# Performance work log

Measured on AMD Instinct MI355X. Metric: run time of the kernel, lower is better.

## Reference

```python
import jax, jax.numpy as jnp
import numpy as np

B, J, D, H, W, AE, GH, NA, EH, L = 64, 20000, 32, 64, 4, 16, 24, 5000, 128, 32


def _ln(x, g=None, b=None, eps=1e-5):
    mu = x.mean(-1, keepdims=True)
    var = jnp.mean((x - mu) ** 2, axis=-1, keepdims=True)
    y = (x - mu) * jax.lax.rsqrt(var + eps)
    if g is not None:
        y = y * g + b
    return y


def setup_inputs():
    key = jax.random.key(0)
    ks = jax.random.split(key, 12)
    def rn(k, shape, s):
        return (jax.random.normal(k, shape) * s).astype(jnp.float32)
    return {
        "x": jax.random.normal(ks[0], (B, J), jnp.float32),
        "mask": jax.random.randint(ks[1], (B, J), 0, 2, jnp.int32),
        "atse_idx": jax.random.randint(ks[2], (J,), 0, NA, jnp.int32),
        "feature_embedding": jax.random.normal(ks[3], (J, D), jnp.float32),
        "atse_embedding": jax.random.normal(ks[4], (NA, AE), jnp.float32),
        "h_W1": rn(ks[5], (1 + D, H), 0.15), "h_b1": jnp.zeros((H,), jnp.float32),
        "h_ln1_g": jnp.ones((H,), jnp.float32), "h_ln1_b": jnp.zeros((H,), jnp.float32),
        "h_W2": rn(ks[6], (H, D), 0.12), "h_b2": jnp.zeros((D,), jnp.float32),
        "h_ln2_g": jnp.ones((D,), jnp.float32), "h_ln2_b": jnp.zeros((D,), jnp.float32),
        "g_W1": rn(ks[7], (D + AE, GH), 0.14), "g_b1": jnp.zeros((GH,), jnp.float32),
        "g_W2": rn(ks[8], (GH, W), 0.2), "g_b2": jnp.zeros((W,), jnp.float32),
        "c_W": rn(ks[9], (W * D, D), 0.09), "c_b": jnp.zeros((D,), jnp.float32),
        "c_ln_g": jnp.ones((D,), jnp.float32), "c_ln_b": jnp.zeros((D,), jnp.float32),
        "e_W1": rn(ks[10], (D, EH), 0.18), "e_b1": jnp.zeros((EH,), jnp.float32),
        "e_W2": rn(ks[11], (EH, 2 * L), 0.09), "e_b2": jnp.zeros((2 * L,), jnp.float32),
    }


def _forward(x, mask, atse_idx, feature_embedding, atse_embedding,
             h_W1, h_b1, h_ln1_g, h_ln1_b, h_W2, h_b2, h_ln2_g, h_ln2_b,
             g_W1, g_b1, g_W2, g_b2, c_W, c_b, c_ln_g, c_ln_b,
             e_W1, e_b1, e_W2, e_b2):
    TEMP = 1.0  # temperature_fixed=True -> scale = temperature_value
    Bv, Jv = x.shape
    Dv = feature_embedding.shape[1]
    # h-layer on all (b, j) pairs; LayerNorm/ReLU are per-row so this equals the
    # per-sample gather version on observed rows (unobserved rows get zero weight below).
    h_in = jnp.concatenate(
        [x[..., None], jnp.broadcast_to(feature_embedding[None], (Bv, Jv, Dv))], axis=-1)
    h = jax.nn.relu(_ln(h_in @ h_W1 + h_b1, h_ln1_g, h_ln1_b))
    h_out = jax.nn.relu(_ln(h @ h_W2 + h_b2, h_ln2_g, h_ln2_b))  # [B, J, D]
    # gate: [h_out | E_atse(j)] -> W head logits
    ae = atse_embedding[atse_idx]  # [J, AE]
    gate_in = jnp.concatenate(
        [h_out, jnp.broadcast_to(ae[None], (Bv, Jv, ae.shape[1]))], axis=-1)
    raw = jax.nn.relu(gate_in @ g_W1 + g_b1) @ g_W2 + g_b2  # [B, J, W]
    logits = jnp.clip(raw * TEMP, -10.0, 10.0)
    obs = mask.astype(bool)
    masked = jnp.where(obs[..., None], logits, -1e9)
    weights = jax.nn.softmax(masked, axis=1)  # softmax over observed junctions per head
    head_sums = jnp.einsum('bjw,bjd->bwd', weights, h_out)  # [B, W, D]
    Wn, Dn = head_sums.shape[1], head_sums.shape[2]
    combined = jax.nn.relu(_ln(head_sums.reshape(Bv, Wn * Dn) @ c_W + c_b, c_ln_g, c_ln_b))
    combined = jnp.where(obs.any(axis=1)[:, None], combined, 0.0)  # empty-mask rows -> zeros
    # encoder_mlp: scvi FCLayers, 2 layers, LayerNorm (no affine) + ReLU each
    e1 = jax.nn.relu(_ln(combined @ e_W1 + e_b1))
    mu_logvar = jax.nn.relu(_ln(e1 @ e_W2 + e_b2))
    mu, logvar = jnp.split(mu_logvar, 2, axis=-1)
    return mu, logvar


def reference(x, mask, atse_idx, feature_embedding, atse_embedding,
              h_W1, h_b1, h_ln1_g, h_ln1_b, h_W2, h_b2, h_ln2_g, h_ln2_b,
              g_W1, g_b1, g_W2, g_b2, c_W, c_b, c_ln_g, c_ln_b,
              e_W1, e_b1, e_W2, e_b2):
    return _forward(x, mask, atse_idx, feature_embedding, atse_embedding,
                    h_W1, h_b1, h_ln1_g, h_ln1_b, h_W2, h_b2, h_ln2_g, h_ln2_b,
                    g_W1, g_b1, g_W2, g_b2, c_W, c_b, c_ln_g, c_ln_b,
                    e_W1, e_b1, e_W2, e_b2)
```

## Files before the change

### kernel.cpp

```cpp
#include <hip/hip_runtime.h>
#include <hip/hip_bf16.h>
#include <math.h>

#define Bv 64
#define Jv 20000
#define NJT 625
#define NBT 8

typedef __attribute__((ext_vector_type(8))) short short8;
typedef __attribute__((ext_vector_type(4))) float f32x4;

union U8 { short8 s; unsigned int u[4]; };

__device__ __forceinline__ unsigned short f2bf(float f) {
  unsigned int u = __float_as_uint(f);
  u += 0x7FFFu + ((u >> 16) & 1u);
  return (unsigned short)(u >> 16);
}
__device__ __forceinline__ unsigned int pkbf(float a, float b) {
  __hip_bfloat162 h = __float22bfloat162_rn(make_float2(a, b));
  union { __hip_bfloat162 h; unsigned int u; } c;
  c.h = h;
  return c.u;
}
__device__ __forceinline__ float bflo(unsigned int u) { return __uint_as_float(u << 16); }
__device__ __forceinline__ float bfhi(unsigned int u) { return __uint_as_float(u & 0xFFFF0000u); }

__global__ __launch_bounds__(256) void pe_fused(
    const float* __restrict__ x, const int* __restrict__ mask,
    const int* __restrict__ atse_idx, const float* __restrict__ fe,
    const float* __restrict__ ae,
    const float* __restrict__ hW1, const float* __restrict__ hb1,
    const float* __restrict__ hl1g, const float* __restrict__ hl1b,
    const float* __restrict__ hW2, const float* __restrict__ hb2,
    const float* __restrict__ hl2g, const float* __restrict__ hl2b,
    const float* __restrict__ gW1, const float* __restrict__ gb1,
    const float* __restrict__ gW2, const float* __restrict__ gb2,
    float* __restrict__ acc_g, float* __restrict__ se_g) {
  __shared__ __align__(16) float s_pg[32 * 68];
  __shared__ __align__(16) float s_ex[32 * 4];
  __shared__ __align__(16) float s_gb[32 * 28 + 16];
  __shared__ __align__(16) float s_pair[256 * 4];
  __shared__ __align__(16) float s_w0[64], s_w0g[64], s_l1g[64], s_l1b[64];
  __shared__ __align__(16) float s_b2[32], s_l2g[32], s_l2b[32];
  __shared__ __align__(16) float s_gb1[24], s_gW2[96];
  __shared__ float s_gb2[4], s_scal[2];
  __shared__ int s_mk[256];
  __shared__ __align__(16) unsigned short s_gW1bf[32 * 24];
  __shared__ __align__(16) unsigned short s_ovl[256 * 34];

  int tid = threadIdx.x;
  int btile = blockIdx.x;
  int jtile = blockIdx.y;
  int J0 = jtile * 32;
  int lane = tid & 63, wv = tid >> 6;
  int li = lane & 15, quad = lane >> 4;

  float* ovlf = (float*)s_ovl;
  float* s_aeo = ovlf + 2048;
  float* s_gW1bo = ovlf + 2688;
  unsigned short* s_h = s_ovl;

  for (int i = tid; i < 2048; i += 256) ovlf[i] = hW2[i];
  for (int i = tid; i < 768; i += 256) s_gW1bf[i] = f2bf(gW1[i]);
  for (int i = tid; i < 384; i += 256) s_gW1bo[i] = gW1[768 + i];
  if (tid < 96) s_gW2[tid] = gW2[tid];
  if (tid < 64) { s_w0[tid] = hW1[tid]; s_l1g[tid] = hl1g[tid]; s_l1b[tid] = hl1b[tid]; }
  if (tid < 32) { s_b2[tid] = hb2[tid]; s_l2g[tid] = hl2g[tid]; s_l2b[tid] = hl2b[tid]; }
  if (tid < 24) s_gb1[tid] = gb1[tid];
  if (tid < 4) s_gb2[tid] = gb2[tid];
  if (tid < 128) s_gb[(tid >> 2) * 28 + 24 + (tid & 3)] = 0.f;
  if (tid >= 128 && tid < 144) s_gb[32 * 28 + (tid - 128)] = 0.f;
  if (tid < 32) {
    int ai = atse_idx[J0 + tid];
    const float4* av = (const float4*)(ae + (size_t)ai * 16);
#pragma unroll
    for (int q = 0; q < 4; ++q) *(float4*)(s_aeo + tid * 20 + q * 4) = av[q];
  }
  __syncthreads();

  {
    U8 bH;
#pragma unroll
    for (int p = 0; p < 4; ++p) {
      float lo = hW1[(1 + quad * 8 + 2 * p) * 64 + wv * 16 + li];
      float hi = hW1[(1 + quad * 8 + 2 * p + 1) * 64 + wv * 16 + li];
      bH.u[p] = pkbf(lo, hi);
    }
    float hb = hb1[wv * 16 + li];
    f32x4 cP;
#pragma unroll
    for (int mt = 0; mt < 2; ++mt) {
      cP[0] = hb; cP[1] = hb; cP[2] = hb; cP[3] = hb;
      const float* fp = fe + (size_t)(J0 + mt * 16 + li) * 32 + quad * 8;
      float4 f0 = *(const float4*)fp;
      float4 f1 = *(const float4*)(fp + 4);
      U8 aF;
      aF.u[0] = pkbf(f0.x, f0.y); aF.u[1] = pkbf(f0.z, f0.w);
      aF.u[2] = pkbf(f1.x, f1.y); aF.u[3] = pkbf(f1.z, f1.w);
      cP = __builtin_amdgcn_mfma_f32_16x16x32_bf16(aF.s, bH.s, cP, 0, 0, 0);
#pragma unroll
      for (int r = 0; r < 4; ++r)
        s_pg[(mt * 16 + quad * 4 + r) * 68 + wv * 16 + li] = cP[r];
    }
  }
  {
    int jp = tid >> 3, ks = tid & 7;
    int c0 = ks * 3;
    float g3[3] = {s_gb1[c0], s_gb1[c0 + 1], s_gb1[c0 + 2]};
#pragma unroll 4
    for (int a = 0; a < 16; ++a) {
      float Av = s_aeo[jp * 20 + a];
      const float* gr = s_gW1bo + a * 24 + c0;
      g3[0] = fmaf(Av, gr[0], g3[0]);
      g3[1] = fmaf(Av, gr[1], g3[1]);
      g3[2] = fmaf(Av, gr[2], g3[2]);
    }
    s_gb[jp * 28 + c0] = g3[0];
    s_gb[jp * 28 + c0 + 1] = g3[1];
    s_gb[jp * 28 + c0 + 2] = g3[2];
  }
  __syncthreads();

  if (tid < 32) {
    float sp = 0.f, qp = 0.f, dwp = 0.f;
#pragma unroll 8
    for (int k = 0; k < 64; ++k) {
      float p = s_pg[tid * 68 + k];
      float w = s_w0[k];
      sp += p;
      qp = fmaf(p, p, qp);
      dwp = fmaf(p, w, dwp);
    }
    ((float4*)s_ex)[tid] = make_float4(sp, qp, dwp, 0.f);
  } else if (tid == 32) {
    float sw = 0.f, qw = 0.f;
    for (int k = 0; k < 64; ++k) {
      float w = s_w0[k];
      sw += w;
      qw = fmaf(w, w, qw);
    }
    s_scal[0] = sw;
    s_scal[1] = qw;
  } else if (tid >= 64 && tid < 128) {
    s_w0g[tid - 64] = s_w0[tid - 64] * s_l1g[tid - 64];
  }
  __syncthreads();

  {
    int jp = tid >> 3, ks = tid & 7;
    float* pp = s_pg + jp * 68 + ks * 8;
    float4 a0 = *(float4*)pp, a1 = *(float4*)(pp + 4);
    float4 g0 = *(float4*)(s_l1g + ks * 8), g1 = *(float4*)(s_l1g + ks * 8 + 4);
    a0.x *= g0.x; a0.y *= g0.y; a0.z *= g0.z; a0.w *= g0.w;
    a1.x *= g1.x; a1.y *= g1.y; a1.z *= g1.z; a1.w *= g1.w;
    *(float4*)pp = a0;
    *(float4*)(pp + 4) = a1;
  }
  short8 bW2[2][2];
#pragma unroll
  for (int kt = 0; kt < 2; ++kt)
#pragma unroll
    for (int nt = 0; nt < 2; ++nt) {
      U8 t;
#pragma unroll
      for (int p = 0; p < 4; ++p) {
        float lo = ovlf[(kt * 32 + quad * 8 + 2 * p) * 32 + nt * 16 + li];
        float hi = ovlf[(kt * 32 + quad * 8 + 2 * p + 1) * 32 + nt * 16 + li];
        t.u[p] = pkbf(lo, hi);
      }
      bW2[kt][nt] = t.s;
    }
  {
    int j = tid >> 3, b = tid & 7;
    size_t off = (size_t)(btile * 8 + b) * Jv + J0 + j;
    float xv = x[off];
    s_mk[tid] = mask[off];
    float4 ex = ((const float4*)s_ex)[j];
    float mu1 = fmaf(xv, s_scal[0], ex.x) * 0.015625f;
    float Et2 = fmaf(xv * xv, s_scal[1], fmaf(2.0f * xv, ex.z, ex.y)) * 0.015625f;
    float rs1 = rsqrtf(fmaxf(Et2 - mu1 * mu1, 0.f) + 1e-5f);
    *(float4*)(s_pair + tid * 4) = make_float4(xv * rs1, rs1, -mu1 * rs1, 0.f);
  }
  __syncthreads();

  {
    f32x4 cd[4][2];
    float b2a = s_b2[li], b2b = s_b2[16 + li];
#pragma unroll
    for (int t = 0; t < 4; ++t) {
      cd[t][0][0] = b2a; cd[t][0][1] = b2a; cd[t][0][2] = b2a; cd[t][0][3] = b2a;
      cd[t][1][0] = b2b; cd[t][1][1] = b2b; cd[t][1][2] = b2b; cd[t][1][3] = b2b;
    }
#pragma unroll
    for (int kt = 0; kt < 2; ++kt) {
      int base = kt * 32 + quad * 8;
      float4 wg0 = *(const float4*)(s_w0g + base);
      float4 wg1 = *(const float4*)(s_w0g + base + 4);
      float4 gg0 = *(const float4*)(s_l1g + base);
      float4 gg1 = *(const float4*)(s_l1g + base + 4);
      float4 bb0 = *(const float4*)(s_l1b + base);
      float4 bb1 = *(const float4*)(s_l1b + base + 4);
      float wg[8] = {wg0.x, wg0.y, wg0.z, wg0.w, wg1.x, wg1.y, wg1.z, wg1.w};
      float gg[8] = {gg0.x, gg0.y, gg0.z, gg0.w, gg1.x, gg1.y, gg1.z, gg1.w};
      float bb[8] = {bb0.x, bb0.y, bb0.z, bb0.w, bb1.x, bb1.y, bb1.z, bb1.w};
#pragma unroll
      for (int t = 0; t < 4; ++t) {
        int mrow = wv * 64 + t * 16 + li;
        float4 pr = *(const float4*)(s_pair + mrow * 4);
        const float* pgp = s_pg + (mrow >> 3) * 68 + base;
        float4 p0 = *(const float4*)pgp;
        float4 p1 = *(const float4*)(pgp + 4);
        float pv[8] = {p0.x, p0.y, p0.z, p0.w, p1.x, p1.y, p1.z, p1.w};
        float av[8];
#pragma unroll
        for (int i = 0; i < 8; ++i)
          av[i] = fmaxf(fmaf(pr.x, wg[i], fmaf(pr.y, pv[i], fmaf(pr.z, gg[i], bb[i]))), 0.f);
        U8 a8;
        a8.u[0] = pkbf(av[0], av[1]); a8.u[1] = pkbf(av[2], av[3]);
        a8.u[2] = pkbf(av[4], av[5]); a8.u[3] = pkbf(av[6], av[7]);
        cd[t][0] = __builtin_amdgcn_mfma_f32_16x16x32_bf16(a8.s, bW2[kt][0], cd[t][0], 0, 0, 0);
        cd[t][1] = __builtin_amdgcn_mfma_f32_16x16x32_bf16(a8.s, bW2[kt][1], cd[t][1], 0, 0, 0);
      }
    }
    float g0 = s_l2g[li], be0 = s_l2b[li];
    float g1v = s_l2g[16 + li], be1 = s_l2b[16 + li];
#pragma unroll
    for (int t = 0; t < 4; ++t) {
      float sum[4], sq[4];
#pragma unroll
      for (int r = 0; r < 4; ++r) {
        float a = cd[t][0][r], b = cd[t][1][r];
        sum[r] = a + b;
        sq[r] = fmaf(a, a, b * b);
      }
#pragma unroll
      for (int off = 1; off < 16; off <<= 1) {
#pragma unroll
        for (int r = 0; r < 4; ++r) {
          sum[r] += __shfl_xor(sum[r], off);
          sq[r] += __shfl_xor(sq[r], off);
        }
      }
#pragma unroll
      for (int r = 0; r < 4; ++r) {
        float mu = sum[r] * 0.03125f;
        float var = sq[r] * 0.03125f - mu * mu;
        float rs2 = rsqrtf(fmaxf(var, 0.f) + 1e-5f);
        int m = wv * 64 + t * 16 + quad * 4 + r;
        float h0 = fmaxf(fmaf((cd[t][0][r] - mu) * rs2, g0, be0), 0.f);
        float h1 = fmaxf(fmaf((cd[t][1][r] - mu) * rs2, g1v, be1), 0.f);
        s_h[m * 34 + li] = f2bf(h0);
        s_h[m * 34 + 16 + li] = f2bf(h1);
      }
    }
  }

  {
    short8 aG0, aG1;
#pragma unroll
    for (int i = 0; i < 8; ++i) {
      int k = quad * 8 + i;
      aG0[i] = (short)s_gW1bf[k * 24 + li];
      aG1[i] = (li < 8) ? (short)s_gW1bf[k * 24 + 16 + li] : (short)0;
    }
    float4 gw4[2][4];
#pragma unroll
    for (int mt = 0; mt < 2; ++mt)
#pragma unroll
      for (int r = 0; r < 4; ++r) {
        int c = mt * 16 + quad * 4 + r;
        gw4[mt][r] = (c < 24) ? ((const float4*)s_gW2)[c]
                              : make_float4(0.f, 0.f, 0.f, 0.f);
      }
#pragma unroll
    for (int nt = 0; nt < 4; ++nt) {
      int m = wv * 64 + nt * 16 + li;
      U8 bu;
      const unsigned short* hp = s_h + m * 34 + quad * 8;
      bu.u[0] = *(const unsigned int*)(hp + 0);
      bu.u[1] = *(const unsigned int*)(hp + 2);
      bu.u[2] = *(const unsigned int*)(hp + 4);
      bu.u[3] = *(const unsigned int*)(hp + 6);
      int j = m >> 3;
      f32x4 c0, c1;
#pragma unroll
      for (int r = 0; r < 4; ++r) {
        c0[r] = s_gb[j * 28 + quad * 4 + r];
        c1[r] = s_gb[j * 28 + 16 + quad * 4 + r];
      }
      c0 = __builtin_amdgcn_mfma_f32_16x16x32_bf16(aG0, bu.s, c0, 0, 0, 0);
      c1 = __builtin_amdgcn_mfma_f32_16x16x32_bf16(aG1, bu.s, c1, 0, 0, 0);
      float r0 = s_gb2[0], r1 = s_gb2[1], r2 = s_gb2[2], r3 = s_gb2[3];
#pragma unroll
      for (int r = 0; r < 4; ++r) {
        float v0 = fmaxf(c0[r], 0.f);
        float v1 = fmaxf(c1[r], 0.f);
        float4 ga = gw4[0][r], gb = gw4[1][r];
        r0 = fmaf(v0, ga.x, fmaf(v1, gb.x, r0));
        r1 = fmaf(v0, ga.y, fmaf(v1, gb.y, r1));
        r2 = fmaf(v0, ga.z, fmaf(v1, gb.z, r2));
        r3 = fmaf(v0, ga.w, fmaf(v1, gb.w, r3));
      }
      r0 += __shfl_xor(r0, 16); r0 += __shfl_xor(r0, 32);
      r1 += __shfl_xor(r1, 16); r1 += __shfl_xor(r1, 32);
      r2 += __shfl_xor(r2, 16); r2 += __shfl_xor(r2, 32);
      r3 += __shfl_xor(r3, 16); r3 += __shfl_xor(r3, 32);
      r0 = fminf(fmaxf(r0, -10.f), 10.f);
      r1 = fminf(fmaxf(r1, -10.f), 10.f);
      r2 = fminf(fmaxf(r2, -10.f), 10.f);
      r3 = fminf(fmaxf(r3, -10.f), 10.f);
      bool act = (s_mk[m] != 0);
      float e0 = act ? __expf(r0 - 10.f) : 0.f;
      float e1 = act ? __expf(r1 - 10.f) : 0.f;
      float e2 = act ? __expf(r2 - 10.f) : 0.f;
      float e3 = act ? __expf(r3 - 10.f) : 0.f;
      if (quad == 0) *(float4*)(s_pair + m * 4) = make_float4(e0, e1, e2, e3);
    }
  }
  __syncthreads();

  {
    const float* s_e2 = s_pair;
#pragma unroll
    for (int bs = 0; bs < 2; ++bs) {
      int b = wv * 2 + bs;
      float ev[8];
      float separt = 0.f;
#pragma unroll
      for (int i = 0; i < 8; ++i) {
        float v = s_e2[((quad * 8 + i) * 8 + b) * 4 + (li & 3)];
        v = (li < 4) ? v : 0.f;
        ev[i] = v;
        separt += v;
      }
      separt += __shfl_xor(separt, 16);
      separt += __shfl_xor(separt, 32);
      U8 a8;
      a8.u[0] = pkbf(ev[0], ev[1]); a8.u[1] = pkbf(ev[2], ev[3]);
      a8.u[2] = pkbf(ev[4], ev[5]); a8.u[3] = pkbf(ev[6], ev[7]);
#pragma unroll
      for (int half = 0; half < 2; ++half) {
        U8 bh;
#pragma unroll
        for (int p = 0; p < 4; ++p) {
          unsigned int lo = s_h[((quad * 8 + 2 * p) * 8 + b) * 34 + half * 16 + li];
          unsigned int hi = s_h[((quad * 8 + 2 * p + 1) * 8 + b) * 34 + half * 16 + li];
          bh.u[p] = lo | (hi << 16);
        }
        f32x4 c = {0.f, 0.f, 0.f, 0.f};
        c = __builtin_amdgcn_mfma_f32_16x16x32_bf16(a8.s, bh.s, c, 0, 0, 0);
        if (quad == 0) {
          float* dst = acc_g + (size_t)(btile * 8 + b) * 128;
#pragma unroll
          for (int r = 0; r < 4; ++r)
            atomicAdd(dst + r * 32 + half * 16 + li, c[r]);
        }
      }
      if (quad == 0 && li < 4)
        atomicAdd(&se_g[(btile * 8 + b) * 4 + li], separt);
    }
  }
}

__global__ __launch_bounds__(64) void pe_tail(
    const float* __restrict__ acc_g, const float* __restrict__ se_g,
    const float* __restrict__ cW, const float* __restrict__ cb,
    const float* __restrict__ clng, const float* __restrict__ clnb,
    const float* __restrict__ eW1, const float* __restrict__ eb1,
    const float* __restrict__ eW2, const float* __restrict__ eb2,
    float* __restrict__ out) {
  int b = blockIdx.x;
  int lane = threadIdx.x;
  __shared__ float s_hs[128], s_comb[32], s_e1[128];

  float se0 = se_g[b * 4 + 0];
  bool empty = !(se0 > 0.0f);
  float inv[4];
#pragma unroll
  for (int w = 0; w < 4; ++w) {
    float sw = se_g[b * 4 + w];
    inv[w] = empty ? 0.0f : 1.0f / sw;
  }
  s_hs[lane] = acc_g[b * 128 + lane] * inv[lane >> 5];
  s_hs[lane + 64] = acc_g[b * 128 + lane + 64] * inv[(lane + 64) >> 5];
  __syncthreads();

  if (lane < 32) {
    float cp = cb[lane];
#pragma unroll 8
    for (int i = 0; i < 128; ++i) cp = fmaf(s_hs[i], cW[i * 32 + lane], cp);
    float ssum = cp;
#pragma unroll
    for (int off = 16; off > 0; off >>= 1) ssum += __shfl_xor(ssum, off, 32);
    float mu = ssum * (1.0f / 32.0f);
    float dd = cp - mu;
    float sq = dd * dd;
#pragma unroll
    for (int off = 16; off > 0; off >>= 1) sq += __shfl_xor(sq, off, 32);
    float rs = rsqrtf(sq * (1.0f / 32.0f) + 1e-5f);
    float comb = fmaxf(fmaf(dd * rs, clng[lane], clnb[lane]), 0.0f);
    if (empty) comb = 0.0f;
    s_comb[lane] = comb;
  }
  __syncthreads();

  float v0 = eb1[lane], v1 = eb1[lane + 64];
#pragma unroll
  for (int i = 0; i < 32; ++i) {
    float c = s_comb[i];
    v0 = fmaf(c, eW1[i * 128 + lane], v0);
    v1 = fmaf(c, eW1[i * 128 + lane + 64], v1);
  }
  float ssum = v0 + v1;
#pragma unroll
  for (int off = 32; off > 0; off >>= 1) ssum += __shfl_xor(ssum, off, 64);
  float mu = ssum * (1.0f / 128.0f);
  float d0 = v0 - mu, d1 = v1 - mu;
  float sq = fmaf(d0, d0, d1 * d1);
#pragma unroll
  for (int off = 32; off > 0; off >>= 1) sq += __shfl_xor(sq, off, 64);
  float rs = rsqrtf(sq * (1.0f / 128.0f) + 1e-5f);
  s_e1[lane] = fmaxf(d0 * rs, 0.0f);
  s_e1[lane + 64] = fmaxf(d1 * rs, 0.0f);
  __syncthreads();

  float v = eb2[lane];
#pragma unroll 8
  for (int i = 0; i < 128; ++i) v = fmaf(s_e1[i], eW2[i * 64 + lane], v);
  ssum = v;
#pragma unroll
  for (int off = 32; off > 0; off >>= 1) ssum += __shfl_xor(ssum, off, 64);
  mu = ssum * (1.0f / 64.0f);
  float dv = v - mu;
  sq = dv * dv;
#pragma unroll
  for (int off = 32; off > 0; off >>= 1) sq += __shfl_xor(sq, off, 64);
  rs = rsqrtf(sq * (1.0f / 64.0f) + 1e-5f);
  float o = fmaxf(dv * rs, 0.0f);
  if (lane < 32)
    out[b * 32 + lane] = o;
  else
    out[Bv * 32 + b * 32 + (lane - 32)] = o;
}

extern "C" void kernel_launch(void* const* d_in, const int* in_sizes, int n_in,
                              void* d_out, int out_size, void* d_ws, size_t ws_size,
                              hipStream_t stream) {
  const float* x    = (const float*)d_in[0];
  const int* mask   = (const int*)d_in[1];
  const int* atse   = (const int*)d_in[2];
  const float* fe   = (const float*)d_in[3];
  const float* ae   = (const float*)d_in[4];
  const float* hW1  = (const float*)d_in[5];
  const float* hb1  = (const float*)d_in[6];
  const float* hl1g = (const float*)d_in[7];
  const float* hl1b = (const float*)d_in[8];
  const float* hW2  = (const float*)d_in[9];
  const float* hb2  = (const float*)d_in[10];
  const float* hl2g = (const float*)d_in[11];
  const float* hl2b = (const float*)d_in[12];
  const float* gW1  = (const float*)d_in[13];
  const float* gb1  = (const float*)d_in[14];
  const float* gW2  = (const float*)d_in[15];
  const float* gb2  = (const float*)d_in[16];
  const float* cW   = (const float*)d_in[17];
  const float* cb   = (const float*)d_in[18];
  const float* clng = (const float*)d_in[19];
  const float* clnb = (const float*)d_in[20];
  const float* eW1  = (const float*)d_in[21];
  const float* eb1  = (const float*)d_in[22];
  const float* eW2  = (const float*)d_in[23];
  const float* eb2  = (const float*)d_in[24];
  float* out = (float*)d_out;

  float* ws = (float*)d_ws;
  float* accg = ws;
  float* seg  = accg + Bv * 128;

  hipMemsetAsync(accg, 0, (Bv * 128 + Bv * 4) * sizeof(float), stream);

  pe_fused<<<dim3(NBT, NJT), dim3(256), 0, stream>>>(
      x, mask, atse, fe, ae, hW1, hb1, hl1g, hl1b, hW2, hb2, hl2g, hl2b,
      gW1, gb1, gW2, gb2, accg, seg);
  pe_tail<<<dim3(Bv), dim3(64), 0, stream>>>(
      accg, seg, cW, cb, clng, clnb, eW1, eb1, eW2, eb2, out);
}
```

Before: 231.1 us.

## Fold atse-embedding gate bias into MFMA and drop shared-memory overlay staging

New measurement: 245.1 us. +6.0%, slower.

```diff
diff --git a/kernel.cpp b/kernel.cpp
--- a/kernel.cpp
+++ b/kernel.cpp
@@ -39,15 +39,17 @@
     float* __restrict__ acc_g, float* __restrict__ se_g) {
   __shared__ __align__(16) float s_pg[32 * 68];
   __shared__ __align__(16) float s_ex[32 * 4];
-  __shared__ __align__(16) float s_gb[32 * 28 + 16];
   __shared__ __align__(16) float s_pair[256 * 4];
   __shared__ __align__(16) float s_w0[64], s_w0g[64], s_l1g[64], s_l1b[64];
   __shared__ __align__(16) float s_b2[32], s_l2g[32], s_l2b[32];
-  __shared__ __align__(16) float s_gb1[24], s_gW2[96];
+  __shared__ __align__(16) float s_gb1p[32];
+  __shared__ __align__(16) float s_gW2[96];
   __shared__ float s_gb2[4], s_scal[2];
   __shared__ int s_mk[256];
   __shared__ __align__(16) unsigned short s_gW1bf[32 * 24];
-  __shared__ __align__(16) unsigned short s_ovl[256 * 34];
+  __shared__ __align__(16) unsigned short s_gW1bbf[16 * 24];
+  __shared__ __align__(16) unsigned short s_aebf[32 * 16];
+  __shared__ __align__(16) unsigned short s_h[256 * 34];
 
   int tid = threadIdx.x;
   int btile = blockIdx.x;
@@ -56,28 +58,24 @@
   int lane = tid & 63, wv = tid >> 6;
   int li = lane & 15, quad = lane >> 4;
 
-  float* ovlf = (float*)s_ovl;
-  float* s_aeo = ovlf + 2048;
-  float* s_gW1bo = ovlf + 2688;
-  unsigned short* s_h = s_ovl;
-
-  for (int i = tid; i < 2048; i += 256) ovlf[i] = hW2[i];
   for (int i = tid; i < 768; i += 256) s_gW1bf[i] = f2bf(gW1[i]);
-  for (int i = tid; i < 384; i += 256) s_gW1bo[i] = gW1[768 + i];
+  for (int i = tid; i < 384; i += 256) s_gW1bbf[i] = f2bf(gW1[768 + i]);
   if (tid < 96) s_gW2[tid] = gW2[tid];
   if (tid < 64) { s_w0[tid] = hW1[tid]; s_l1g[tid] = hl1g[tid]; s_l1b[tid] = hl1b[tid]; }
   if (tid < 32) { s_b2[tid] = hb2[tid]; s_l2g[tid] = hl2g[tid]; s_l2b[tid] = hl2b[tid]; }
-  if (tid < 24) s_gb1[tid] = gb1[tid];
+  if (tid < 32) s_gb1p[tid] = (tid < 24) ? gb1[tid] : 0.f;
   if (tid < 4) s_gb2[tid] = gb2[tid];
-  if (tid < 128) s_gb[(tid >> 2) * 28 + 24 + (tid & 3)] = 0.f;
-  if (tid >= 128 && tid < 144) s_gb[32 * 28 + (tid - 128)] = 0.f;
   if (tid < 32) {
     int ai = atse_idx[J0 + tid];
     const float4* av = (const float4*)(ae + (size_t)ai * 16);
-#pragma unroll
-    for (int q = 0; q < 4; ++q) *(float4*)(s_aeo + tid * 20 + q * 4) = av[q];
-  }
-  __syncthreads();
+    unsigned int* dst = (unsigned int*)s_aebf + tid * 8;
+#pragma unroll
+    for (int q = 0; q < 4; ++q) {
+      float4 v = av[q];
+      dst[q * 2] = pkbf(v.x, v.y);
+      dst[q * 2 + 1] = pkbf(v.z, v.w);
+    }
+  }
 
   {
     U8 bH;
@@ -104,22 +102,6 @@
         s_pg[(mt * 16 + quad * 4 + r) * 68 + wv * 16 + li] = cP[r];
     }
   }
-  {
-    int jp = tid >> 3, ks = tid & 7;
-    int c0 = ks * 3;
-    float g3[3] = {s_gb1[c0], s_gb1[c0 + 1], s_gb1[c0 + 2]};
-#pragma unroll 4
-    for (int a = 0; a < 16; ++a) {
-      float Av = s_aeo[jp * 20 + a];
-      const float* gr = s_gW1bo + a * 24 + c0;
-      g3[0] = fmaf(Av, gr[0], g3[0]);
-      g3[1] = fmaf(Av, gr[1], g3[1]);
-      g3[2] = fmaf(Av, gr[2], g3[2]);
-    }
-    s_gb[jp * 28 + c0] = g3[0];
-    s_gb[jp * 28 + c0 + 1] = g3[1];
-    s_gb[jp * 28 + c0 + 2] = g3[2];
-  }
   __syncthreads();
 
   if (tid < 32) {
@@ -147,6 +129,7 @@
   }
   __syncthreads();
 
+
   {
     int jp = tid >> 3, ks = tid & 7;
     float* pp = s_pg + jp * 68 + ks * 8;
@@ -165,8 +148,8 @@
       U8 t;
 #pragma unroll
       for (int p = 0; p < 4; ++p) {
-        float lo = ovlf[(kt * 32 + quad * 8 + 2 * p) * 32 + nt * 16 + li];
-        float hi = ovlf[(kt * 32 + quad * 8 + 2 * p + 1) * 32 + nt * 16 + li];
+        float lo = hW2[(kt * 32 + quad * 8 + 2 * p) * 32 + nt * 16 + li];
+        float hi = hW2[(kt * 32 + quad * 8 + 2 * p + 1) * 32 + nt * 16 + li];
         t.u[p] = pkbf(lo, hi);
       }
       bW2[kt][nt] = t.s;
@@ -182,7 +165,6 @@
     float rs1 = rsqrtf(fmaxf(Et2 - mu1 * mu1, 0.f) + 1e-5f);
     *(float4*)(s_pair + tid * 4) = make_float4(xv * rs1, rs1, -mu1 * rs1, 0.f);
   }
-  __syncthreads();
 
   {
     f32x4 cd[4][2];
@@ -257,12 +239,20 @@
   }
 
   {
-    short8 aG0, aG1;
+    short8 aG0, aG1, aB0, aB1;
 #pragma unroll
     for (int i = 0; i < 8; ++i) {
       int k = quad * 8 + i;
       aG0[i] = (short)s_gW1bf[k * 24 + li];
       aG1[i] = (li < 8) ? (short)s_gW1bf[k * 24 + 16 + li] : (short)0;
+      aB0[i] = (k < 16) ? (short)s_gW1bbf[k * 24 + li] : (short)0;
+      aB1[i] = (k < 16 && li < 8) ? (short)s_gW1bbf[k * 24 + 16 + li] : (short)0;
+    }
+    float gbc0[4], gbc1[4];
+#pragma unroll
+    for (int r = 0; r < 4; ++r) {
+      gbc0[r] = s_gb1p[quad * 4 + r];
+      gbc1[r] = s_gb1p[16 + quad * 4 + r];
     }
     float4 gw4[2][4];
 #pragma unroll
@@ -283,12 +273,16 @@
       bu.u[2] = *(const unsigned int*)(hp + 4);
       bu.u[3] = *(const unsigned int*)(hp + 6);
       int j = m >> 3;
+      U8 bu2;
+      const unsigned int* aep = (const unsigned int*)s_aebf + j * 8;
+#pragma unroll
+      for (int p = 0; p < 4; ++p)
+        bu2.u[p] = (quad < 2) ? aep[quad * 4 + p] : 0u;
       f32x4 c0, c1;
 #pragma unroll
-      for (int r = 0; r < 4; ++r) {
-        c0[r] = s_gb[j * 28 + quad * 4 + r];
-        c1[r] = s_gb[j * 28 + 16 + quad * 4 + r];
-      }
+      for (int r = 0; r < 4; ++r) { c0[r] = gbc0[r]; c1[r] = gbc1[r]; }
+      c0 = __builtin_amdgcn_mfma_f32_16x16x32_bf16(aB0, bu2.s, c0, 0, 0, 0);
+      c1 = __builtin_amdgcn_mfma_f32_16x16x32_bf16(aB1, bu2.s, c1, 0, 0, 0);
       c0 = __builtin_amdgcn_mfma_f32_16x16x32_bf16(aG0, bu.s, c0, 0, 0, 0);
       c1 = __builtin_amdgcn_mfma_f32_16x16x32_bf16(aG1, bu.s, c1, 0, 0, 0);
       float r0 = s_gb2[0], r1 = s_gb2[1], r2 = s_gb2[2], r3 = s_gb2[3];
```
